# Performance work log

Hardware: AMD Instinct MI355X
Metric: run time of the kernel (lower is better)

Reference implementation:

```python
import jax, jax.numpy as jnp
import numpy as np

B, S, DIN, E, H, L, F, DOUT = 16, 1024, 64, 512, 8, 6, 2048, 2
DH = E // H
EPS = 1e-5

def _make_pe(n, d):
    # replicates PositionalEncoding buffer: pe[pos, 2i]=sin, pe[pos,2i+1]=cos
    pos = np.arange(n, dtype=np.float32)[:, None]
    div = np.exp(np.arange(0, d, 2, dtype=np.float32) * (-np.log(10000.0) / d))
    pe = np.zeros((n, d), dtype=np.float32)
    pe[:, 0::2] = np.sin(pos * div)
    pe[:, 1::2] = np.cos(pos * div)
    return pe

def _layernorm(x, g, b):
    m = jnp.mean(x, axis=-1, keepdims=True)
    v = jnp.mean((x - m) ** 2, axis=-1, keepdims=True)
    return (x - m) * jax.lax.rsqrt(v + EPS) * g + b

def setup_inputs() -> dict:
    key = jax.random.key(0)
    ks = iter(jax.random.split(key, 40))
    def xavier(k, shape):
        fan_in, fan_out = shape[-2], shape[-1]
        lim = np.sqrt(6.0 / (fan_in + fan_out)).astype(np.float32)
        return jax.random.uniform(k, shape, jnp.float32, -lim, lim)
    inp = {}
    inp['x'] = jax.random.normal(next(ks), (B, S, DIN), jnp.float32)
    inp['Win'] = xavier(next(ks), (DIN, E)); inp['b_in'] = jnp.zeros((E,), jnp.float32)
    # pe[:x.size(0)] with batch-first x -> slice first B positions, broadcast over seq
    inp['pe'] = jnp.asarray(_make_pe(B, E))[:, None, :]  # [B,1,E]
    inp['Wq'] = xavier(next(ks), (L, E, E)); inp['bq'] = jnp.zeros((L, E), jnp.float32)
    inp['Wk'] = xavier(next(ks), (L, E, E)); inp['bk'] = jnp.zeros((L, E), jnp.float32)
    inp['Wv'] = xavier(next(ks), (L, E, E)); inp['bv'] = jnp.zeros((L, E), jnp.float32)
    inp['Wo'] = xavier(next(ks), (L, E, E)); inp['bo'] = jnp.zeros((L, E), jnp.float32)
    inp['g1'] = jnp.ones((L, E), jnp.float32); inp['be1'] = jnp.zeros((L, E), jnp.float32)
    inp['W1'] = xavier(next(ks), (L, E, F)); inp['b1'] = jnp.zeros((L, F), jnp.float32)
    inp['W2'] = xavier(next(ks), (L, F, E)); inp['b2'] = jnp.zeros((L, E), jnp.float32)
    inp['g2'] = jnp.ones((L, E), jnp.float32); inp['be2'] = jnp.zeros((L, E), jnp.float32)
    inp['gf'] = jnp.ones((E,), jnp.float32); inp['bef'] = jnp.zeros((E,), jnp.float32)
    inp['Wout'] = xavier(next(ks), (E, DOUT)); inp['bout'] = jnp.zeros((DOUT,), jnp.float32)
    return inp

def reference(x, Win, b_in, pe, Wq, bq, Wk, bk, Wv, bv, Wo, bo,
              g1, be1, W1, b1, W2, b2, g2, be2, gf, bef, Wout, bout):
    scale = 1.0 / np.sqrt(DH).astype(np.float32)
    h = x @ Win + b_in + pe  # [B,S,E], pe broadcast over seq (replicates source bug)
    for i in range(L):
        resid = h
        q = (h @ Wq[i] + bq[i]).reshape(B, S, H, DH)
        k = (h @ Wk[i] + bk[i]).reshape(B, S, H, DH)
        v = (h @ Wv[i] + bv[i]).reshape(B, S, H, DH)
        scores = jnp.einsum('bqhd,bkhd->bhqk', q, k) * scale
        attn = jax.nn.softmax(scores, axis=-1)
        o = jnp.einsum('bhqk,bkhd->bqhd', attn, v).reshape(B, S, E)
        o = o @ Wo[i] + bo[i]
        a = _layernorm(o + resid, g1[i], be1[i])
        f = jax.nn.relu(a @ W1[i] + b1[i]) @ W2[i] + b2[i]
        h = _layernorm(f + a, g2[i], be2[i])
    out = _layernorm(h, gf, bef) @ Wout + bout
    return out
```

## Files before the change

kernel.cpp:

```cpp
#include <hip/hip_runtime.h>
#include <hip/hip_bf16.h>

typedef __bf16 bf16_t;
typedef __bf16 bf16x8 __attribute__((ext_vector_type(8)));
typedef __bf16 bf16x4 __attribute__((ext_vector_type(4)));
typedef float f32x4 __attribute__((ext_vector_type(4)));

#define B_ 16
#define S_ 1024
#define E_ 512
#define H_ 8
#define DH_ 64
#define L_ 6
#define F_ 2048
#define M_ (B_ * S_)

#define EXP2F(x) __builtin_amdgcn_exp2f(x)

#define GLOAD_LDS16(gsrc, ldst) \
    __builtin_amdgcn_global_load_lds((const __attribute__((address_space(1))) void*)(gsrc), \
                                     (__attribute__((address_space(3))) void*)(ldst), 16, 0, 0)

__global__ void cast_bf16_kernel(const float* __restrict__ src, bf16_t* __restrict__ dst, int n) {
    int i = (blockIdx.x * 256 + threadIdx.x) * 4;
    if (i + 3 < n) {
        f32x4 v = *(const f32x4*)&src[i];
        #pragma unroll
        for (int j = 0; j < 4; ++j) dst[i + j] = (bf16_t)v[j];
    }
}

__global__ void castT_kernel(const float* __restrict__ src, bf16_t* __restrict__ dst,
                             int K, int N, size_t dstZ) {
    __shared__ bf16_t tile[32][33];
    size_t so = (size_t)blockIdx.z * K * N;
    size_t dofs = (size_t)blockIdx.z * dstZ;
    int k0 = blockIdx.y * 32, n0 = blockIdx.x * 32;
    int tx = threadIdx.x, ty = threadIdx.y;
    for (int i = ty; i < 32; i += 8)
        tile[i][tx] = (bf16_t)src[so + (size_t)(k0 + i) * N + n0 + tx];
    __syncthreads();
    for (int i = ty; i < 32; i += 8)
        dst[dofs + (size_t)(n0 + i) * K + k0 + tx] = tile[tx][i];
}

__global__ void pack_bias_kernel(const float* __restrict__ bq, const float* __restrict__ bk,
                                 const float* __restrict__ bv, float* __restrict__ dst) {
    int i = blockIdx.x * 256 + threadIdx.x;
    if (i >= L_ * 1536) return;
    int l = i / 1536, c = i % 1536;
    float v = (c < 512) ? bq[l * 512 + c] : (c < 1024 ? bk[l * 512 + c - 512] : bv[l * 512 + c - 1024]);
    dst[i] = v;
}

template<int EPI, bool RELU>
__launch_bounds__(256, 2)
__global__ void gemm_kernel(const bf16_t* __restrict__ A, const bf16_t* __restrict__ BT,
                            const float* __restrict__ bias, bf16_t* __restrict__ out16,
                            const float* __restrict__ auxf,
                            int M, int N, int K)
{
    __shared__ bf16_t As[2][128][32];
    __shared__ bf16_t Bs[2][128][32];
    const int tid = threadIdx.x;
    const int lane = tid & 63;
    const int w = tid >> 6;
    const int wm = w >> 1, wn = w & 1;
    const int m0 = blockIdx.x * 128, n0 = blockIdx.y * 128;
    const int l15 = lane & 15, lg = lane >> 4;

    const int srow = w * 32 + (lane >> 2);
    const int scol = (lane & 3) * 8;
    const bf16_t* Ab = A + (size_t)(m0 + srow) * K + scol;
    const bf16_t* Bb = BT + (size_t)(n0 + srow) * K + scol;

    f32x4 acc[4][4] = {};
    const int nt = K >> 5;

    #define STAGE(buf, t) do { \
        size_t ko_ = (size_t)(t) * 32; \
        _Pragma("unroll") \
        for (int j_ = 0; j_ < 2; ++j_) { \
            GLOAD_LDS16(Ab + (size_t)j_ * 16 * K + ko_, &As[buf][w * 32 + j_ * 16][0]); \
            GLOAD_LDS16(Bb + (size_t)j_ * 16 * K + ko_, &Bs[buf][w * 32 + j_ * 16][0]); \
        } } while (0)

    STAGE(0, 0);
    __syncthreads();
    int cur = 0;
    for (int t = 0; t < nt; ++t) {
        if (t + 1 < nt) STAGE(cur ^ 1, t + 1);
        bf16x8 af[4], bfr[4];
        #pragma unroll
        for (int m = 0; m < 4; ++m) af[m] = *(const bf16x8*)&As[cur][wm * 64 + m * 16 + l15][lg * 8];
        #pragma unroll
        for (int n = 0; n < 4; ++n) bfr[n] = *(const bf16x8*)&Bs[cur][wn * 64 + n * 16 + l15][lg * 8];
        __builtin_amdgcn_s_setprio(1);
        #pragma unroll
        for (int m = 0; m < 4; ++m)
            #pragma unroll
            for (int n = 0; n < 4; ++n)
                acc[m][n] = __builtin_amdgcn_mfma_f32_16x16x32_bf16(af[m], bfr[n], acc[m][n], 0, 0, 0);
        __builtin_amdgcn_s_setprio(0);
        __syncthreads();
        cur ^= 1;
    }
    #undef STAGE

    #pragma unroll
    for (int m = 0; m < 4; ++m) {
        #pragma unroll
        for (int n = 0; n < 4; ++n) {
            int col = n0 + wn * 64 + n * 16 + l15;
            float bv = bias[col];
            #pragma unroll
            for (int r = 0; r < 4; ++r) {
                int row = m0 + wm * 64 + m * 16 + lg * 4 + r;
                float v = acc[m][n][r] + bv;
                if (EPI == 1) v += auxf[(size_t)(row >> 10) * E_ + col];
                if (RELU) v = fmaxf(v, 0.f);
                out16[(size_t)row * N + col] = (bf16_t)v;
            }
        }
    }
}

template<int EPI, bool RELU>
__launch_bounds__(512, 2)
__global__ void gemm2_kernel(const bf16_t* __restrict__ A, const bf16_t* __restrict__ BT,
                             const float* __restrict__ bias, bf16_t* __restrict__ out16,
                             const bf16_t* __restrict__ auxb,
                             bf16_t* __restrict__ outk, bf16_t* __restrict__ outv,
                             int M, int N, int K)
{
    __shared__ bf16_t AB[3][12288];
    const int tid = threadIdx.x;
    const int lane = tid & 63;
    const int w = tid >> 6;
    const int wr = w >> 2, wc = w & 3;
    const int m0 = blockIdx.x * 128, n0 = blockIdx.y * 256;
    const int l15 = lane & 15, lg = lane >> 4;

    const int srow = w * 16 + (lane >> 2);
    const int scol = ((lane & 3) ^ ((lane >> 3) & 3)) * 8;
    const int cswz = (lg ^ ((l15 >> 1) & 3)) * 8;
    const bf16_t* Ab  = A  + (size_t)(m0 + srow) * K + scol;
    const bf16_t* Bb0 = BT + (size_t)(n0 + srow) * K + scol;
    const bf16_t* Bb1 = BT + (size_t)(n0 + 128 + srow) * K + scol;

    f32x4 acc[4][4] = {};
    const int nt = K >> 5;

    #define STAGE3(kt, buf) do { \
        size_t ko_ = (size_t)(kt) * 32; \
        GLOAD_LDS16(Ab  + ko_, &AB[buf][w * 512]); \
        GLOAD_LDS16(Bb0 + ko_, &AB[buf][4096 + w * 512]); \
        GLOAD_LDS16(Bb1 + ko_, &AB[buf][8192 + w * 512]); \
    } while (0)

    STAGE3(0, 0);
    STAGE3(1, 1);
    asm volatile("s_waitcnt vmcnt(3)" ::: "memory");
    __builtin_amdgcn_s_barrier();

    int bc = 0, bs = 2;
    int t = 0;
    for (; t + 2 < nt; ++t) {
        bf16x8 af[4], bf[4];
        #pragma unroll
        for (int m = 0; m < 4; ++m)
            af[m] = *(const bf16x8*)&AB[bc][(wr * 64 + m * 16 + l15) * 32 + cswz];
        #pragma unroll
        for (int n = 0; n < 4; ++n)
            bf[n] = *(const bf16x8*)&AB[bc][4096 + (wc * 64 + n * 16 + l15) * 32 + cswz];
        STAGE3(t + 2, bs);
        asm volatile("s_waitcnt vmcnt(3)" ::: "memory");
        __builtin_amdgcn_s_barrier();
        __builtin_amdgcn_s_setprio(1);
        #pragma unroll
        for (int m = 0; m < 4; ++m)
            #pragma unroll
            for (int n = 0; n < 4; ++n)
                acc[m][n] = __builtin_amdgcn_mfma_f32_16x16x32_bf16(af[m], bf[n], acc[m][n], 0, 0, 0);
        __builtin_amdgcn_s_setprio(0);
        bc = (bc == 2) ? 0 : bc + 1;
        bs = (bs == 2) ? 0 : bs + 1;
    }
    for (; t < nt; ++t) {
        bf16x8 af[4], bf[4];
        #pragma unroll
        for (int m = 0; m < 4; ++m)
            af[m] = *(const bf16x8*)&AB[bc][(wr * 64 + m * 16 + l15) * 32 + cswz];
        #pragma unroll
        for (int n = 0; n < 4; ++n)
            bf[n] = *(const bf16x8*)&AB[bc][4096 + (wc * 64 + n * 16 + l15) * 32 + cswz];
        asm volatile("s_waitcnt vmcnt(0)" ::: "memory");
        __builtin_amdgcn_s_barrier();
        __builtin_amdgcn_s_setprio(1);
        #pragma unroll
        for (int m = 0; m < 4; ++m)
            #pragma unroll
            for (int n = 0; n < 4; ++n)
                acc[m][n] = __builtin_amdgcn_mfma_f32_16x16x32_bf16(af[m], bf[n], acc[m][n], 0, 0, 0);
        __builtin_amdgcn_s_setprio(0);
        bc = (bc == 2) ? 0 : bc + 1;
    }
    #undef STAGE3

    #pragma unroll
    for (int m = 0; m < 4; ++m) {
        #pragma unroll
        for (int n = 0; n < 4; ++n) {
            int col = n0 + wc * 64 + n * 16 + l15;
            float bv = bias[col];
            #pragma unroll
            for (int r = 0; r < 4; ++r) {
                int row = m0 + wr * 64 + m * 16 + lg * 4 + r;
                float v = acc[m][n][r] + bv;
                if (EPI == 0) {
                    if (RELU) v = fmaxf(v, 0.f);
                    out16[(size_t)row * N + col] = (bf16_t)v;
                } else if (EPI == 2) {
                    v += (float)auxb[(size_t)row * N + col];
                    out16[(size_t)row * N + col] = (bf16_t)v;
                }
            }
        }
    }
    (void)outk; (void)outv;
}

template<int EPI, bool RELU>
__launch_bounds__(256, 3)
__global__ void gemm2b_kernel(const bf16_t* __restrict__ A, const bf16_t* __restrict__ BT,
                              const float* __restrict__ bias, bf16_t* __restrict__ out16,
                              const bf16_t* __restrict__ auxb,
                              bf16_t* __restrict__ outk, bf16_t* __restrict__ outv,
                              int M, int N, int K)
{
    __shared__ bf16_t As[3][128][32];
    __shared__ bf16_t Bs[3][128][32];
    const int tid = threadIdx.x;
    const int lane = tid & 63;
    const int w = tid >> 6;
    const int wm = w >> 1, wn = w & 1;
    const int m0 = blockIdx.x * 128, n0 = blockIdx.y * 128;
    const int l15 = lane & 15, lg = lane >> 4;

    const int srow = lane >> 2;
    const int scol = ((lane & 3) ^ ((lane >> 3) & 3)) * 8;
    const int cswz = (lg ^ ((l15 >> 1) & 3)) * 8;
    const bf16_t* Ab = A  + (size_t)(m0 + w * 32 + srow) * K + scol;
    const bf16_t* Bb = BT + (size_t)(n0 + w * 32 + srow) * K + scol;

    f32x4 acc[4][4] = {};
    const int nt = K >> 5;

    #define STAGE4(kt, buf) do { \
        size_t ko_ = (size_t)(kt) * 32; \
        GLOAD_LDS16(Ab + ko_,                  &As[buf][w * 32][0]); \
        GLOAD_LDS16(Ab + (size_t)16 * K + ko_, &As[buf][w * 32 + 16][0]); \
        GLOAD_LDS16(Bb + ko_,                  &Bs[buf][w * 32][0]); \
        GLOAD_LDS16(Bb + (size_t)16 * K + ko_, &Bs[buf][w * 32 + 16][0]); \
    } while (0)

    STAGE4(0, 0);
    STAGE4(1, 1);
    asm volatile("s_waitcnt vmcnt(4)" ::: "memory");
    __builtin_amdgcn_s_barrier();

    int bc = 0, bs = 2;
    int t = 0;
    for (; t + 2 < nt; ++t) {
        bf16x8 af[4], bf[4];
        #pragma unroll
        for (int m = 0; m < 4; ++m)
            af[m] = *(const bf16x8*)&As[bc][wm * 64 + m * 16 + l15][cswz];
        #pragma unroll
        for (int n = 0; n < 4; ++n)
            bf[n] = *(const bf16x8*)&Bs[bc][wn * 64 + n * 16 + l15][cswz];
        STAGE4(t + 2, bs);
        asm volatile("s_waitcnt vmcnt(4)" ::: "memory");
        __builtin_amdgcn_s_barrier();
        __builtin_amdgcn_s_setprio(1);
        #pragma unroll
        for (int m = 0; m < 4; ++m)
            #pragma unroll
            for (int n = 0; n < 4; ++n)
                acc[m][n] = __builtin_amdgcn_mfma_f32_16x16x32_bf16(af[m], bf[n], acc[m][n], 0, 0, 0);
        __builtin_amdgcn_s_setprio(0);
        bc = (bc == 2) ? 0 : bc + 1;
        bs = (bs == 2) ? 0 : bs + 1;
    }
    for (; t < nt; ++t) {
        bf16x8 af[4], bf[4];
        #pragma unroll
        for (int m = 0; m < 4; ++m)
            af[m] = *(const bf16x8*)&As[bc][wm * 64 + m * 16 + l15][cswz];
        #pragma unroll
        for (int n = 0; n < 4; ++n)
            bf[n] = *(const bf16x8*)&Bs[bc][wn * 64 + n * 16 + l15][cswz];
        asm volatile("s_waitcnt vmcnt(0)" ::: "memory");
        __builtin_amdgcn_s_barrier();
        __builtin_amdgcn_s_setprio(1);
        #pragma unroll
        for (int m = 0; m < 4; ++m)
            #pragma unroll
            for (int n = 0; n < 4; ++n)
                acc[m][n] = __builtin_amdgcn_mfma_f32_16x16x32_bf16(af[m], bf[n], acc[m][n], 0, 0, 0);
        __builtin_amdgcn_s_setprio(0);
        bc = (bc == 2) ? 0 : bc + 1;
    }
    #undef STAGE4

    #pragma unroll
    for (int m = 0; m < 4; ++m) {
        #pragma unroll
        for (int n = 0; n < 4; ++n) {
            int col = n0 + wn * 64 + n * 16 + l15;
            float bv = bias[col];
            if (EPI == 4 && col >= 1024) {
                int row0 = m0 + wm * 64 + m * 16 + lg * 4;
                int b = row0 >> 10, s0 = row0 & 1023;
                int vcol = col - 1024;
                bf16x4 pk;
                #pragma unroll
                for (int r = 0; r < 4; ++r) pk[r] = (bf16_t)(acc[m][n][r] + bv);
                *(bf16x4*)&outv[((size_t)(b * H_ + (vcol >> 6)) * DH_ + (vcol & 63)) * S_ + s0] = pk;
            } else {
                #pragma unroll
                for (int r = 0; r < 4; ++r) {
                    int row = m0 + wm * 64 + m * 16 + lg * 4 + r;
                    float v = acc[m][n][r] + bv;
                    if (EPI == 0) {
                        if (RELU) v = fmaxf(v, 0.f);
                        out16[(size_t)row * N + col] = (bf16_t)v;
                    } else if (EPI == 2) {
                        v += (float)auxb[(size_t)row * N + col];
                        out16[(size_t)row * N + col] = (bf16_t)v;
                    } else {
                        if (col < 512) out16[(size_t)row * 512 + col] = (bf16_t)v;
                        else           outk[(size_t)row * 512 + (col - 512)] = (bf16_t)v;
                    }
                }
            }
        }
    }
}

__launch_bounds__(512, 4)
__global__ void attn_kernel(const bf16_t* __restrict__ q, const bf16_t* __restrict__ k,
                            const bf16_t* __restrict__ vt, bf16_t* __restrict__ o)
{
    const int id = blockIdx.x;
    const int rest = id >> 3;
    const int qb = rest & 3;
    const int bh = (id & 7) * 16 + (rest >> 2);
    const int b = bh >> 3, h = bh & 7;
    const int tid = threadIdx.x, lane = tid & 63, w = tid >> 6;
    const int l15 = lane & 15, lg = lane >> 4;
    const int q0 = qb * 256 + w * 32;

    __shared__ bf16_t Ks[3][64 * 64];
    __shared__ bf16_t Vs[3][64 * 64];
    __shared__ char psh_all[8][4096];
    char* psh = psh_all[w];
    const int swz = (l15 & 7) << 4;

    const bf16_t* kb = k + (size_t)b * S_ * E_ + h * DH_;
    const bf16_t* vb = vt + (size_t)(b * H_ + h) * DH_ * S_;

    const int r8 = lane >> 3, c8 = lane & 7;

    #define STAGE_ATTN(buf, kk0) do { \
        int row_ = w * 8 + r8; \
        int ch_ = (c8 ^ r8) * 8; \
        GLOAD_LDS16(kb + (size_t)((kk0) + row_) * E_ + ch_, &Ks[buf][(w * 8) * 64]); \
        GLOAD_LDS16(vb + (size_t)row_ * S_ + (kk0) + ch_, &Vs[buf][(w * 8) * 64]); \
    } while (0)

    bf16x8 aq[2][2];
    #pragma unroll
    for (int m = 0; m < 2; ++m) {
        const size_t qoff = (size_t)(b * S_ + q0 + m * 16 + l15) * E_ + h * DH_;
        aq[m][0] = *(const bf16x8*)&q[qoff + lg * 8];
        aq[m][1] = *(const bf16x8*)&q[qoff + 32 + lg * 8];
    }

    float lrow[2] = {0.f, 0.f};
    f32x4 accO[2][4] = {};

    const float sc = 0.125f * 1.44269504f;
    const int c0 = (lg ^ (l15 & 7)) * 8;
    const int c1 = c0 ^ 32;

    const int NT = S_ / 64;
    STAGE_ATTN(0, 0);
    STAGE_ATTN(1, 64);
    asm volatile("s_waitcnt vmcnt(2)" ::: "memory");
    __builtin_amdgcn_s_barrier();

    int bc = 0, bs = 2;
    for (int it = 0; it < NT; ++it) {
        if (it + 2 < NT) STAGE_ATTN(bs, (it + 2) * 64);

        f32x4 sf[2][4];
        #pragma unroll
        for (int n = 0; n < 4; ++n) {
            const int r = n * 16 + l15;
            bf16x8 bk0 = *(const bf16x8*)&Ks[bc][r * 64 + c0];
            bf16x8 bk1 = *(const bf16x8*)&Ks[bc][r * 64 + c1];
            __builtin_amdgcn_s_setprio(1);
            #pragma unroll
            for (int m = 0; m < 2; ++m) {
                f32x4 s = {};
                s = __builtin_amdgcn_mfma_f32_16x16x32_bf16(bk0, aq[m][0], s, 0, 0, 0);
                s = __builtin_amdgcn_mfma_f32_16x16x32_bf16(bk1, aq[m][1], s, 0, 0, 0);
                sf[m][n] = s;
            }
            __builtin_amdgcn_s_setprio(0);
        }

        #pragma unroll
        for (int m = 0; m < 2; ++m) {
            float ps = 0.f;
            #pragma unroll
            for (int n = 0; n < 4; ++n) {
                bf16x4 pw;
                #pragma unroll
                for (int r = 0; r < 4; ++r) {
                    float pv = EXP2F(fmaf(sf[m][n][r], sc, -16.f));
                    ps += pv;
                    pw[r] = (bf16_t)pv;
                }
                *(bf16x4*)(psh + (m * 16 + l15) * 128 + ((n * 32 + lg * 8) ^ swz)) = pw;
            }
            ps += __shfl_xor(ps, 16, 64);
            ps += __shfl_xor(ps, 32, 64);
            lrow[m] += ps;
        }
        asm volatile("" ::: "memory");

        bf16x8 pa[2][2];
        #pragma unroll
        for (int m = 0; m < 2; ++m)
            #pragma unroll
            for (int kk = 0; kk < 2; ++kk)
                pa[m][kk] = *(const bf16x8*)(psh + (m * 16 + l15) * 128 + ((kk * 64 + lg * 16) ^ swz));
        bf16x8 vv[4];
        #pragma unroll
        for (int dt = 0; dt < 4; ++dt)
            vv[dt] = *(const bf16x8*)&Vs[bc][(dt * 16 + l15) * 64 + c0];
        __builtin_amdgcn_s_setprio(1);
        #pragma unroll
        for (int dt = 0; dt < 4; ++dt)
            #pragma unroll
            for (int m = 0; m < 2; ++m)
                accO[m][dt] = __builtin_amdgcn_mfma_f32_16x16x32_bf16(vv[dt], pa[m][0], accO[m][dt], 0, 0, 0);
        __builtin_amdgcn_s_setprio(0);
        #pragma unroll
        for (int dt = 0; dt < 4; ++dt)
            vv[dt] = *(const bf16x8*)&Vs[bc][(dt * 16 + l15) * 64 + c1];
        __builtin_amdgcn_s_setprio(1);
        #pragma unroll
        for (int dt = 0; dt < 4; ++dt)
            #pragma unroll
            for (int m = 0; m < 2; ++m)
                accO[m][dt] = __builtin_amdgcn_mfma_f32_16x16x32_bf16(vv[dt], pa[m][1], accO[m][dt], 0, 0, 0);
        __builtin_amdgcn_s_setprio(0);

        if (it + 1 < NT) {
            if (it + 2 < NT) asm volatile("s_waitcnt vmcnt(2)" ::: "memory");
            else             asm volatile("s_waitcnt vmcnt(0)" ::: "memory");
            __builtin_amdgcn_s_barrier();
        }
        bc = (bc == 2) ? 0 : bc + 1;
        bs = (bs == 2) ? 0 : bs + 1;
    }
    #undef STAGE_ATTN

    #pragma unroll
    for (int m = 0; m < 2; ++m) {
        float rl = 1.f / lrow[m];
        #pragma unroll
        for (int dt = 0; dt < 4; ++dt) {
            bf16x4 ov;
            #pragma unroll
            for (int r = 0; r < 4; ++r) ov[r] = (bf16_t)(accO[m][dt][r] * rl);
            *(bf16x4*)&o[(size_t)(b * S_ + q0 + m * 16 + l15) * E_ + h * DH_ + dt * 16 + lg * 4] = ov;
        }
    }
}

__launch_bounds__(256)
__global__ void ln_kernel(const bf16_t* __restrict__ in, const float* __restrict__ g,
                          const float* __restrict__ be, bf16_t* __restrict__ out)
{
    int row = blockIdx.x * 4 + (threadIdx.x >> 6);
    int lane = threadIdx.x & 63;
    bf16x8 v = *(const bf16x8*)&in[(size_t)row * E_ + lane * 8];
    float x[8];
    #pragma unroll
    for (int j = 0; j < 8; ++j) x[j] = (float)v[j];
    float s = 0.f;
    #pragma unroll
    for (int j = 0; j < 8; ++j) s += x[j];
    #pragma unroll
    for (int off = 32; off >= 1; off >>= 1) s += __shfl_xor(s, off, 64);
    float mean = s * (1.f / E_);
    float vs = 0.f;
    #pragma unroll
    for (int j = 0; j < 8; ++j) { float d = x[j] - mean; vs += d * d; }
    #pragma unroll
    for (int off = 32; off >= 1; off >>= 1) vs += __shfl_xor(vs, off, 64);
    float rstd = rsqrtf(vs * (1.f / E_) + 1e-5f);
    bf16x8 y;
    #pragma unroll
    for (int j = 0; j < 8; ++j) {
        int col = lane * 8 + j;
        y[j] = (bf16_t)((x[j] - mean) * rstd * g[col] + be[col]);
    }
    *(bf16x8*)&out[(size_t)row * E_ + lane * 8] = y;
}

__launch_bounds__(256)
__global__ void final_kernel(const bf16_t* __restrict__ in, const float* __restrict__ g,
                             const float* __restrict__ be, const float* __restrict__ Wout,
                             const float* __restrict__ bout, float* __restrict__ out)
{
    int row = blockIdx.x * 4 + (threadIdx.x >> 6);
    int lane = threadIdx.x & 63;
    bf16x8 v = *(const bf16x8*)&in[(size_t)row * E_ + lane * 8];
    float x[8];
    #pragma unroll
    for (int j = 0; j < 8; ++j) x[j] = (float)v[j];
    float s = 0.f;
    #pragma unroll
    for (int j = 0; j < 8; ++j) s += x[j];
    #pragma unroll
    for (int off = 32; off >= 1; off >>= 1) s += __shfl_xor(s, off, 64);
    float mean = s * (1.f / E_);
    float vs = 0.f;
    #pragma unroll
    for (int j = 0; j < 8; ++j) { float d = x[j] - mean; vs += d * d; }
    #pragma unroll
    for (int off = 32; off >= 1; off >>= 1) vs += __shfl_xor(vs, off, 64);
    float rstd = rsqrtf(vs * (1.f / E_) + 1e-5f);
    float p0 = 0.f, p1 = 0.f;
    #pragma unroll
    for (int j = 0; j < 8; ++j) {
        int col = lane * 8 + j;
        float y = (x[j] - mean) * rstd * g[col] + be[col];
        p0 += y * Wout[col * 2 + 0];
        p1 += y * Wout[col * 2 + 1];
    }
    #pragma unroll
    for (int off = 32; off >= 1; off >>= 1) { p0 += __shfl_xor(p0, off, 64); p1 += __shfl_xor(p1, off, 64); }
    if (lane == 0) {
        out[(size_t)row * 2 + 0] = p0 + bout[0];
        out[(size_t)row * 2 + 1] = p1 + bout[1];
    }
}

extern "C" void kernel_launch(void* const* d_in, const int* in_sizes, int n_in,
                              void* d_out, int out_size, void* d_ws, size_t ws_size,
                              hipStream_t stream)
{
    (void)in_sizes; (void)n_in; (void)out_size;
    const float* x    = (const float*)d_in[0];
    const float* Win  = (const float*)d_in[1];
    const float* b_in = (const float*)d_in[2];
    const float* pe   = (const float*)d_in[3];
    const float* Wq   = (const float*)d_in[4];
    const float* bq   = (const float*)d_in[5];
    const float* Wk   = (const float*)d_in[6];
    const float* bk   = (const float*)d_in[7];
    const float* Wv   = (const float*)d_in[8];
    const float* bv   = (const float*)d_in[9];
    const float* Wo   = (const float*)d_in[10];
    const float* bo   = (const float*)d_in[11];
    const float* g1   = (const float*)d_in[12];
    const float* be1  = (const float*)d_in[13];
    const float* W1   = (const float*)d_in[14];
    const float* b1   = (const float*)d_in[15];
    const float* W2   = (const float*)d_in[16];
    const float* b2   = (const float*)d_in[17];
    const float* g2   = (const float*)d_in[18];
    const float* be2  = (const float*)d_in[19];
    const float* gf   = (const float*)d_in[20];
    const float* bef  = (const float*)d_in[21];
    const float* Wout = (const float*)d_in[22];
    const float* bout = (const float*)d_in[23];

    char* p = (char*)d_ws;
    auto take = [&](size_t bytes) { char* r = p; p += (bytes + 255) & ~(size_t)255; return r; };

    bf16_t* xb    = (bf16_t*)take((size_t)M_ * 64 * 2);
    bf16_t* WinT  = (bf16_t*)take((size_t)E_ * 64 * 2);
    bf16_t* WqkvT = (bf16_t*)take((size_t)L_ * 1536 * E_ * 2);
    bf16_t* WoT   = (bf16_t*)take((size_t)L_ * E_ * E_ * 2);
    bf16_t* W1T   = (bf16_t*)take((size_t)L_ * E_ * F_ * 2);
    bf16_t* W2T   = (bf16_t*)take((size_t)L_ * E_ * F_ * 2);
    float*  bqkv  = (float*)take((size_t)L_ * 1536 * 4);
    bf16_t* hb16  = (bf16_t*)take((size_t)M_ * E_ * 2);
    bf16_t* qb16  = (bf16_t*)take((size_t)M_ * E_ * 2);
    bf16_t* kb16  = (bf16_t*)take((size_t)M_ * E_ * 2);
    bf16_t* vtb   = (bf16_t*)take((size_t)M_ * E_ * 2);
    bf16_t* ob16  = (bf16_t*)take((size_t)M_ * E_ * 2);
    bf16_t* tb16  = (bf16_t*)take((size_t)M_ * E_ * 2);
    bf16_t* ab16  = (bf16_t*)take((size_t)M_ * E_ * 2);
    bf16_t* f1b   = qb16;

    if ((size_t)(p - (char*)d_ws) > ws_size) return;

    cast_bf16_kernel<<<dim3(M_ * 64 / 4 / 256), dim3(256), 0, stream>>>(x, xb, M_ * 64);
    castT_kernel<<<dim3(E_ / 32, 64 / 32, 1), dim3(32, 8), 0, stream>>>(Win, WinT, 64, E_, 0);
    castT_kernel<<<dim3(E_ / 32, E_ / 32, L_), dim3(32, 8), 0, stream>>>(
        Wq, WqkvT + (size_t)0 * E_, E_, E_, (size_t)1536 * E_);
    castT_kernel<<<dim3(E_ / 32, E_ / 32, L_), dim3(32, 8), 0, stream>>>(
        Wk, WqkvT + (size_t)512 * E_, E_, E_, (size_t)1536 * E_);
    castT_kernel<<<dim3(E_ / 32, E_ / 32, L_), dim3(32, 8), 0, stream>>>(
        Wv, WqkvT + (size_t)1024 * E_, E_, E_, (size_t)1536 * E_);
    castT_kernel<<<dim3(E_ / 32, E_ / 32, L_), dim3(32, 8), 0, stream>>>(
        Wo, WoT, E_, E_, (size_t)E_ * E_);
    castT_kernel<<<dim3(F_ / 32, E_ / 32, L_), dim3(32, 8), 0, stream>>>(
        W1, W1T, E_, F_, (size_t)E_ * F_);
    castT_kernel<<<dim3(E_ / 32, F_ / 32, L_), dim3(32, 8), 0, stream>>>(
        W2, W2T, F_, E_, (size_t)E_ * F_);
    pack_bias_kernel<<<dim3((L_ * 1536 + 255) / 256), dim3(256), 0, stream>>>(bq, bk, bv, bqkv);

    gemm_kernel<1, false><<<dim3(M_ / 128, E_ / 128), dim3(256), 0, stream>>>(
        xb, WinT, b_in, hb16, pe, M_, E_, 64);

    for (int i = 0; i < L_; ++i) {
        const bf16_t* WqkvTi = WqkvT + (size_t)i * 1536 * E_;
        const bf16_t* WoTi   = WoT + (size_t)i * E_ * E_;
        const bf16_t* W1Ti   = W1T + (size_t)i * E_ * F_;
        const bf16_t* W2Ti   = W2T + (size_t)i * E_ * F_;

        gemm2b_kernel<4, false><<<dim3(M_ / 128, 1536 / 128), dim3(256), 0, stream>>>(
            hb16, WqkvTi, bqkv + (size_t)i * 1536, qb16, nullptr, kb16, vtb, M_, 1536, E_);
        attn_kernel<<<dim3(512), dim3(512), 0, stream>>>(qb16, kb16, vtb, ob16);
        gemm2b_kernel<2, false><<<dim3(M_ / 128, E_ / 128), dim3(256), 0, stream>>>(
            ob16, WoTi, bo + i * E_, tb16, hb16, nullptr, nullptr, M_, E_, E_);
        ln_kernel<<<dim3(M_ / 4), dim3(256), 0, stream>>>(tb16, g1 + i * E_, be1 + i * E_, ab16);
        gemm2_kernel<0, true><<<dim3(M_ / 128, F_ / 256), dim3(512), 0, stream>>>(
            ab16, W1Ti, b1 + i * F_, f1b, nullptr, nullptr, nullptr, M_, F_, E_);
        gemm2b_kernel<2, false><<<dim3(M_ / 128, E_ / 128), dim3(256), 0, stream>>>(
            f1b, W2Ti, b2 + i * E_, tb16, ab16, nullptr, nullptr, M_, E_, F_);
        ln_kernel<<<dim3(M_ / 4), dim3(256), 0, stream>>>(tb16, g2 + i * E_, be2 + i * E_, hb16);
    }

    final_kernel<<<dim3(M_ / 4), dim3(256), 0, stream>>>(hb16, gf, bef, Wout, bout, (float*)d_out);
}
```

Before: 1.167 ms.

## Enlarge GEMM tiles to 256x256, remap blocks XCD-aware, consolidate GEMM kernels

Replaces the 128x128 256-thread GEMM with a 512-thread 256x256-tile kernel for the QKV and FFN1 projections. The Wo and FFN2 projections move to the 128x256 kernel, which now runs with a 1D grid. Block indices are remapped so consecutive tiles land on the same XCD (index mod 8), aiming for better L2 reuse. The larger tiles raise arithmetic intensity per LDS load, at the cost of more registers, fewer blocks and possible wave-quantization effects on the 1D grids.

```diff
diff --git a/kernel.cpp b/kernel.cpp
--- a/kernel.cpp
+++ b/kernel.cpp
@@ -126,19 +126,20 @@
 }
 
 template<int EPI, bool RELU>
-__launch_bounds__(512, 2)
+__launch_bounds__(512, 4)
 __global__ void gemm2_kernel(const bf16_t* __restrict__ A, const bf16_t* __restrict__ BT,
                              const float* __restrict__ bias, bf16_t* __restrict__ out16,
                              const bf16_t* __restrict__ auxb,
-                             bf16_t* __restrict__ outk, bf16_t* __restrict__ outv,
-                             int M, int N, int K)
+                             int M, int N, int K, int gy)
 {
     __shared__ bf16_t AB[3][12288];
     const int tid = threadIdx.x;
     const int lane = tid & 63;
     const int w = tid >> 6;
     const int wr = w >> 2, wc = w & 3;
-    const int m0 = blockIdx.x * 128, n0 = blockIdx.y * 256;
+    const int nblk8 = (int)gridDim.x >> 3;
+    const int orig = (blockIdx.x & 7) * nblk8 + (blockIdx.x >> 3);
+    const int m0 = (orig / gy) * 128, n0 = (orig % gy) * 256;
     const int l15 = lane & 15, lg = lane >> 4;
 
     const int srow = w * 16 + (lane >> 2);
@@ -227,24 +228,23 @@
             }
         }
     }
-    (void)outk; (void)outv;
 }
 
 template<int EPI, bool RELU>
-__launch_bounds__(256, 3)
-__global__ void gemm2b_kernel(const bf16_t* __restrict__ A, const bf16_t* __restrict__ BT,
-                              const float* __restrict__ bias, bf16_t* __restrict__ out16,
-                              const bf16_t* __restrict__ auxb,
-                              bf16_t* __restrict__ outk, bf16_t* __restrict__ outv,
-                              int M, int N, int K)
+__launch_bounds__(512, 2)
+__global__ void gemm4_kernel(const bf16_t* __restrict__ A, const bf16_t* __restrict__ BT,
+                             const float* __restrict__ bias, bf16_t* __restrict__ out16,
+                             bf16_t* __restrict__ outk, bf16_t* __restrict__ outv,
+                             int M, int N, int K, int gy)
 {
-    __shared__ bf16_t As[3][128][32];
-    __shared__ bf16_t Bs[3][128][32];
+    __shared__ bf16_t AB[3][16384];
     const int tid = threadIdx.x;
     const int lane = tid & 63;
     const int w = tid >> 6;
-    const int wm = w >> 1, wn = w & 1;
-    const int m0 = blockIdx.x * 128, n0 = blockIdx.y * 128;
+    const int wr = w >> 2, wc = w & 3;
+    const int nblk8 = (int)gridDim.x >> 3;
+    const int orig = (blockIdx.x & 7) * nblk8 + (blockIdx.x >> 3);
+    const int m0 = (orig / gy) * 256, n0 = (orig % gy) * 256;
     const int l15 = lane & 15, lg = lane >> 4;
 
     const int srow = lane >> 2;
@@ -253,15 +253,15 @@
     const bf16_t* Ab = A  + (size_t)(m0 + w * 32 + srow) * K + scol;
     const bf16_t* Bb = BT + (size_t)(n0 + w * 32 + srow) * K + scol;
 
-    f32x4 acc[4][4] = {};
+    f32x4 acc[8][4] = {};
     const int nt = K >> 5;
 
     #define STAGE4(kt, buf) do { \
         size_t ko_ = (size_t)(kt) * 32; \
-        GLOAD_LDS16(Ab + ko_,                  &As[buf][w * 32][0]); \
-        GLOAD_LDS16(Ab + (size_t)16 * K + ko_, &As[buf][w * 32 + 16][0]); \
-        GLOAD_LDS16(Bb + ko_,                  &Bs[buf][w * 32][0]); \
-        GLOAD_LDS16(Bb + (size_t)16 * K + ko_, &Bs[buf][w * 32 + 16][0]); \
+        GLOAD_LDS16(Ab + ko_,                  &AB[buf][(w * 32) * 32]); \
+        GLOAD_LDS16(Ab + (size_t)16 * K + ko_, &AB[buf][(w * 32 + 16) * 32]); \
+        GLOAD_LDS16(Bb + ko_,                  &AB[buf][8192 + (w * 32) * 32]); \
+        GLOAD_LDS16(Bb + (size_t)16 * K + ko_, &AB[buf][8192 + (w * 32 + 16) * 32]); \
     } while (0)
 
     STAGE4(0, 0);
@@ -272,19 +272,19 @@
     int bc = 0, bs = 2;
     int t = 0;
     for (; t + 2 < nt; ++t) {
-        bf16x8 af[4], bf[4];
-        #pragma unroll
-        for (int m = 0; m < 4; ++m)
-            af[m] = *(const bf16x8*)&As[bc][wm * 64 + m * 16 + l15][cswz];
+        bf16x8 af[8], bf[4];
+        #pragma unroll
+        for (int m = 0; m < 8; ++m)
+            af[m] = *(const bf16x8*)&AB[bc][(wr * 128 + m * 16 + l15) * 32 + cswz];
         #pragma unroll
         for (int n = 0; n < 4; ++n)
-            bf[n] = *(const bf16x8*)&Bs[bc][wn * 64 + n * 16 + l15][cswz];
+            bf[n] = *(const bf16x8*)&AB[bc][8192 + (wc * 64 + n * 16 + l15) * 32 + cswz];
         STAGE4(t + 2, bs);
         asm volatile("s_waitcnt vmcnt(4)" ::: "memory");
         __builtin_amdgcn_s_barrier();
         __builtin_amdgcn_s_setprio(1);
         #pragma unroll
-        for (int m = 0; m < 4; ++m)
+        for (int m = 0; m < 8; ++m)
             #pragma unroll
             for (int n = 0; n < 4; ++n)
                 acc[m][n] = __builtin_amdgcn_mfma_f32_16x16x32_bf16(af[m], bf[n], acc[m][n], 0, 0, 0);
@@ -293,18 +293,18 @@
         bs = (bs == 2) ? 0 : bs + 1;
     }
     for (; t < nt; ++t) {
-        bf16x8 af[4], bf[4];
-        #pragma unroll
-        for (int m = 0; m < 4; ++m)
-            af[m] = *(const bf16x8*)&As[bc][wm * 64 + m * 16 + l15][cswz];
+        bf16x8 af[8], bf[4];
+        #pragma unroll
+        for (int m = 0; m < 8; ++m)
+            af[m] = *(const bf16x8*)&AB[bc][(wr * 128 + m * 16 + l15) * 32 + cswz];
         #pragma unroll
         for (int n = 0; n < 4; ++n)
-            bf[n] = *(const bf16x8*)&Bs[bc][wn * 64 + n * 16 + l15][cswz];
+            bf[n] = *(const bf16x8*)&AB[bc][8192 + (wc * 64 + n * 16 + l15) * 32 + cswz];
         asm volatile("s_waitcnt vmcnt(0)" ::: "memory");
         __builtin_amdgcn_s_barrier();
         __builtin_amdgcn_s_setprio(1);
         #pragma unroll
-        for (int m = 0; m < 4; ++m)
+        for (int m = 0; m < 8; ++m)
             #pragma unroll
             for (int n = 0; n < 4; ++n)
                 acc[m][n] = __builtin_amdgcn_mfma_f32_16x16x32_bf16(af[m], bf[n], acc[m][n], 0, 0, 0);
@@ -314,13 +314,13 @@
     #undef STAGE4
 
     #pragma unroll
-    for (int m = 0; m < 4; ++m) {
+    for (int m = 0; m < 8; ++m) {
         #pragma unroll
         for (int n = 0; n < 4; ++n) {
-            int col = n0 + wn * 64 + n * 16 + l15;
+            int col = n0 + wc * 64 + n * 16 + l15;
             float bv = bias[col];
             if (EPI == 4 && col >= 1024) {
-                int row0 = m0 + wm * 64 + m * 16 + lg * 4;
+                int row0 = m0 + wr * 128 + m * 16 + lg * 4;
                 int b = row0 >> 10, s0 = row0 & 1023;
                 int vcol = col - 1024;
                 bf16x4 pk;
@@ -330,13 +330,10 @@
             } else {
                 #pragma unroll
                 for (int r = 0; r < 4; ++r) {
-                    int row = m0 + wm * 64 + m * 16 + lg * 4 + r;
+                    int row = m0 + wr * 128 + m * 16 + lg * 4 + r;
                     float v = acc[m][n][r] + bv;
                     if (EPI == 0) {
                         if (RELU) v = fmaxf(v, 0.f);
-                        out16[(size_t)row * N + col] = (bf16_t)v;
-                    } else if (EPI == 2) {
-                        v += (float)auxb[(size_t)row * N + col];
                         out16[(size_t)row * N + col] = (bf16_t)v;
                     } else {
                         if (col < 512) out16[(size_t)row * 512 + col] = (bf16_t)v;
@@ -638,16 +635,16 @@
         const bf16_t* W1Ti   = W1T + (size_t)i * E_ * F_;
         const bf16_t* W2Ti   = W2T + (size_t)i * E_ * F_;
 
-        gemm2b_kernel<4, false><<<dim3(M_ / 128, 1536 / 128), dim3(256), 0, stream>>>(
-            hb16, WqkvTi, bqkv + (size_t)i * 1536, qb16, nullptr, kb16, vtb, M_, 1536, E_);
+        gemm4_kernel<4, false><<<dim3(384), dim3(512), 0, stream>>>(
+            hb16, WqkvTi, bqkv + (size_t)i * 1536, qb16, kb16, vtb, M_, 1536, E_, 6);
         attn_kernel<<<dim3(512), dim3(512), 0, stream>>>(qb16, kb16, vtb, ob16);
-        gemm2b_kernel<2, false><<<dim3(M_ / 128, E_ / 128), dim3(256), 0, stream>>>(
-            ob16, WoTi, bo + i * E_, tb16, hb16, nullptr, nullptr, M_, E_, E_);
+        gemm2_kernel<2, false><<<dim3(256), dim3(512), 0, stream>>>(
+            ob16, WoTi, bo + i * E_, tb16, hb16, M_, E_, E_, 2);
         ln_kernel<<<dim3(M_ / 4), dim3(256), 0, stream>>>(tb16, g1 + i * E_, be1 + i * E_, ab16);
-        gemm2_kernel<0, true><<<dim3(M_ / 128, F_ / 256), dim3(512), 0, stream>>>(
-            ab16, W1Ti, b1 + i * F_, f1b, nullptr, nullptr, nullptr, M_, F_, E_);
-        gemm2b_kernel<2, false><<<dim3(M_ / 128, E_ / 128), dim3(256), 0, stream>>>(
-            f1b, W2Ti, b2 + i * E_, tb16, ab16, nullptr, nullptr, M_, E_, F_);
+        gemm4_kernel<0, true><<<dim3(512), dim3(512), 0, stream>>>(
+            ab16, W1Ti, b1 + i * F_, f1b, nullptr, nullptr, M_, F_, E_, 8);
+        gemm2_kernel<2, false><<<dim3(256), dim3(512), 0, stream>>>(
+            f1b, W2Ti, b2 + i * E_, tb16, ab16, M_, E_, F_, 2);
         ln_kernel<<<dim3(M_ / 4), dim3(256), 0, stream>>>(tb16, g2 + i * E_, be2 + i * E_, hb16);
     }
 
```

Result: slower. 1.195 ms (+2.4%).
